# Performance work log

Hardware: AMD Instinct MI355X
Metric: run time of the kernel (lower is better)

The kernel has to match this reference:

```python
import jax, jax.numpy as jnp
import numpy as np

# module config (matches init_kwargs)
NUM_COL_HEADS = 4
NUM_ROW_HEADS = 4
EMBED_COL_DIM = 64
EMBED_ROW_DIM = 64
HEAD_COL = EMBED_COL_DIM // NUM_COL_HEADS  # 16
HEAD_ROW = EMBED_ROW_DIM // NUM_ROW_HEADS  # 16
SCALE = (HEAD_COL * HEAD_ROW) ** (-0.5)


def matrix_mul(x, u, v):
    # 'nm,blnd,dk->blmk'
    return jnp.einsum('nm,blnd,dk->blmk', u, x, v)


def setup_inputs() -> dict:
    key = jax.random.key(0)
    k1, k2, k3, k4, k5 = jax.random.split(key, 5)
    B, L, C, R = 2, 2048, 64, 64
    x = jax.random.normal(k1, (B, L, C, R), dtype=jnp.float32)
    qkv_u = jax.random.uniform(k2, (C, EMBED_COL_DIM), dtype=jnp.float32)
    qkv_v = jax.random.uniform(k3, (R, EMBED_ROW_DIM * 3), dtype=jnp.float32)
    proj_u = jax.random.uniform(k4, (EMBED_COL_DIM, C), dtype=jnp.float32)
    proj_v = jax.random.uniform(k5, (EMBED_ROW_DIM, R), dtype=jnp.float32)
    return {"x": x, "qkv_u": qkv_u, "qkv_v": qkv_v, "proj_u": proj_u, "proj_v": proj_v}


def reference(x, qkv_u, qkv_v, proj_u, proj_v):
    B, L, C, R = x.shape
    # bilinear QKV projection: [B,L,embed_col,3*embed_row]
    qkv = matrix_mul(x, qkv_u, qkv_v)
    qkv = qkv.reshape(B, L, 3, NUM_COL_HEADS, HEAD_COL, NUM_ROW_HEADS, HEAD_ROW)
    qkv = qkv.transpose(2, 0, 3, 5, 1, 4, 6)  # [3,B,Mc,Mr,L,Hc,Hw]
    q, k, v = qkv[0], qkv[1], qkv[2]
    # attention over combined (head_col, head_row) feature axes
    attn = jnp.einsum('bmnihw,bmnjhw->bmnij', q, k)
    attn = jax.nn.softmax(attn / SCALE, axis=-1)  # note: divides by scale, as in source
    out = jnp.einsum('bmnij,bmnjhw->bmnihw', attn, v)
    out = out.transpose(0, 3, 1, 4, 2, 5).reshape(B, L, EMBED_COL_DIM, EMBED_ROW_DIM)
    out = matrix_mul(out, proj_u, proj_v)
    return out
```

## Files before the change

kernel.cpp:

```cpp
#include <hip/hip_runtime.h>
#include <hip/hip_fp16.h>

typedef _Float16 f16x8 __attribute__((ext_vector_type(8)));
typedef _Float16 f16x4 __attribute__((ext_vector_type(4)));
typedef float f32x4 __attribute__((ext_vector_type(4)));


__device__ __forceinline__ void stage16(const _Float16* g, _Float16* l) {
  __builtin_amdgcn_global_load_lds(
      (const __attribute__((address_space(1))) void*)g,
      (__attribute__((address_space(3))) void*)l, 16, 0, 0);
}

__device__ __forceinline__ unsigned int pk2(float a, float b) {
  union { _Float16 h[2]; unsigned int u; } x;
  x.h[0] = (_Float16)a; x.h[1] = (_Float16)b;
  return x.u;
}

struct hl16 { _Float16 h, l; };
__device__ __forceinline__ hl16 split_f16(float v) {
  hl16 r;
  r.h = (_Float16)v;
  r.l = (_Float16)(v - (float)r.h);
  return r;
}

__global__ __launch_bounds__(256) void qkv_kernel(
    const float* __restrict__ x, const float* __restrict__ u,
    const float* __restrict__ v, _Float16* __restrict__ Q,
    _Float16* __restrict__ K, _Float16* __restrict__ V) {
  __shared__ _Float16 sm[24576];
  _Float16* xs_hi = sm;
  _Float16* xs_lo = sm + 4096;
  _Float16* us_hi = sm + 8192;
  _Float16* us_lo = sm + 12288;
  _Float16* Ts_hi = sm + 16384;
  _Float16* Ts_lo = sm + 20480;
  _Float16* vc_hi = sm;
  _Float16* vc_lo = sm + 7680;
  _Float16* qk16 = sm;
  const int bl = blockIdx.x;
  const int b = bl >> 11, l = bl & 2047;
  const int t = threadIdx.x;
  const int w = t >> 6, lane = t & 63;
  const int l15 = lane & 15, quad = lane >> 4;

  {
    const int d = t & 63, wq = t >> 6;
#pragma unroll
    for (int rr = 0; rr < 2; ++rr) {
      const int n0 = wq * 8 + rr * 32;
      f16x8 xh, xl, uh, ul;
#pragma unroll
      for (int j = 0; j < 8; ++j) {
        hl16 sx = split_f16(x[((size_t)bl << 12) + (n0 + j) * 64 + d]);
        hl16 su = split_f16(u[(n0 + j) * 64 + d]);
        xh[j] = sx.h; xl[j] = sx.l;
        uh[j] = su.h; ul[j] = su.l;
      }
      const int un = ((n0 >> 3) ^ (d & 7)) << 3;
      *(f16x8*)(xs_hi + (d << 6) + un) = xh;
      *(f16x8*)(xs_lo + (d << 6) + un) = xl;
      *(f16x8*)(us_hi + (d << 6) + un) = uh;
      *(f16x8*)(us_lo + (d << 6) + un) = ul;
    }
  }
  __syncthreads();

  {
    f32x4 dacc[4];
#pragma unroll
    for (int mt = 0; mt < 4; ++mt) dacc[mt] = (f32x4){0.f, 0.f, 0.f, 0.f};
    const int d = (w << 4) | l15;
#pragma unroll
    for (int ks = 0; ks < 2; ++ks) {
      const int ug = (((ks * 4 + quad) ^ (d & 7)) << 3);
      f16x8 bh = *(const f16x8*)(xs_hi + (d << 6) + ug);
      f16x8 blo = *(const f16x8*)(xs_lo + (d << 6) + ug);
#pragma unroll
      for (int mt = 0; mt < 4; ++mt) {
        const int m = (mt << 4) | l15;
        const int um = (((ks * 4 + quad) ^ (m & 7)) << 3);
        f16x8 ah = *(const f16x8*)(us_hi + (m << 6) + um);
        f16x8 al = *(const f16x8*)(us_lo + (m << 6) + um);
        dacc[mt] = __builtin_amdgcn_mfma_f32_16x16x32_f16(ah, bh, dacc[mt], 0, 0, 0);
        dacc[mt] = __builtin_amdgcn_mfma_f32_16x16x32_f16(ah, blo, dacc[mt], 0, 0, 0);
        dacc[mt] = __builtin_amdgcn_mfma_f32_16x16x32_f16(al, bh, dacc[mt], 0, 0, 0);
      }
    }
#pragma unroll
    for (int mt = 0; mt < 4; ++mt) {
#pragma unroll
      for (int r = 0; r < 4; ++r) {
        const int m = (mt << 4) | (quad << 2) | r;
        const int dd = (w << 4) | l15;
        const int off = (m << 6) + ((((dd >> 3) ^ (m & 7)) << 3) | (dd & 7));
        hl16 st = split_f16(dacc[mt][r]);
        Ts_hi[off] = st.h;
        Ts_lo[off] = st.l;
      }
    }
  }
  __syncthreads();

  f32x4 cacc[4][3];
#pragma unroll
  for (int mt = 0; mt < 4; ++mt)
#pragma unroll
    for (int kt = 0; kt < 3; ++kt) cacc[mt][kt] = (f32x4){0.f, 0.f, 0.f, 0.f};

  for (int chk = 0; chk < 2; ++chk) {
#pragma unroll
    for (int rr = 0; rr < 3; ++rr) {
      const int c768 = t + 256 * rr;
      const int k = c768 >> 2, sg = c768 & 3;
      f16x8 vh, vl;
#pragma unroll
      for (int j = 0; j < 8; ++j) {
        hl16 sv = split_f16(v[(chk * 32 + sg * 8 + j) * 192 + k]);
        vh[j] = sv.h; vl[j] = sv.l;
      }
      *(f16x8*)(vc_hi + k * 40 + sg * 8) = vh;
      *(f16x8*)(vc_lo + k * 40 + sg * 8) = vl;
    }
    __syncthreads();
    f16x8 ah[4], al[4];
#pragma unroll
    for (int mt = 0; mt < 4; ++mt) {
      const int m = (mt << 4) | l15;
      const int off = (m << 6) + (((chk * 4 + quad) ^ (m & 7)) << 3);
      ah[mt] = *(const f16x8*)(Ts_hi + off);
      al[mt] = *(const f16x8*)(Ts_lo + off);
    }
#pragma unroll
    for (int kt = 0; kt < 3; ++kt) {
      const int k = w * 48 + kt * 16 + l15;
      f16x8 bh = *(const f16x8*)(vc_hi + k * 40 + quad * 8);
      f16x8 blo = *(const f16x8*)(vc_lo + k * 40 + quad * 8);
#pragma unroll
      for (int mt = 0; mt < 4; ++mt) {
        cacc[mt][kt] = __builtin_amdgcn_mfma_f32_16x16x32_f16(ah[mt], bh, cacc[mt][kt], 0, 0, 0);
        cacc[mt][kt] = __builtin_amdgcn_mfma_f32_16x16x32_f16(ah[mt], blo, cacc[mt][kt], 0, 0, 0);
        cacc[mt][kt] = __builtin_amdgcn_mfma_f32_16x16x32_f16(al[mt], bh, cacc[mt][kt], 0, 0, 0);
      }
    }
    __syncthreads();
  }

#pragma unroll
  for (int mt = 0; mt < 4; ++mt)
#pragma unroll
    for (int kt = 0; kt < 3; ++kt) {
      const int k = w * 48 + kt * 16 + l15;
#pragma unroll
      for (int r = 0; r < 4; ++r) {
        const int m = (mt << 4) | (quad << 2) | r;
        qk16[m * 192 + k] = (_Float16)cacc[mt][kt][r];
      }
    }
  __syncthreads();

#pragma unroll
  for (int s = 0; s < 3; ++s) {
    const int rho = t + 256 * s;
    const int m = rho / 12, rem = rho - m * 12;
    const int k64 = rem >> 2, mr = rem & 3;
    const int chf = 3 * m + k64;
    const int t3 = chf >> 6, ch = chf & 63;
    const int f0 = (ch & 15) << 4;
    const int h = (b << 4) | ((ch >> 4) << 2) | mr;
    const _Float16* src = qk16 + m * 192 + k64 * 64 + mr * 16;
    f16x8 a0 = *(const f16x8*)src;
    f16x8 a1 = *(const f16x8*)(src + 8);
    _Float16* base = (t3 == 0) ? Q : (t3 == 1) ? K : V;
    _Float16* dst = base + (((size_t)h * 2048 + l) << 8) + f0;
    *(f16x8*)dst = a0;
    *(f16x8*)(dst + 8) = a1;
  }
}

__global__ __launch_bounds__(256) void vtrans_kernel(
    const _Float16* __restrict__ V, _Float16* __restrict__ Vt) {
  __shared__ _Float16 tb[64 * 72];
  const int bid = blockIdx.x;
  const int h = bid >> 7;
  const int lt = (bid >> 2) & 31;
  const int ft = bid & 3;
  const int l0 = lt << 6, f0 = ft << 6;
  const int t = threadIdx.x;
  const int r = t >> 2, s = (t & 3) << 4;
  const _Float16* src = V + (((size_t)h * 2048 + l0 + r) << 8) + f0 + s;
  *(f16x8*)(tb + r * 72 + s) = *(const f16x8*)src;
  *(f16x8*)(tb + r * 72 + s + 8) = *(const f16x8*)(src + 8);
  __syncthreads();
  _Float16 buf[16];
#pragma unroll
  for (int j = 0; j < 16; ++j) buf[j] = tb[(s + j) * 72 + r];
  _Float16* dst = Vt + (((size_t)(h << 8) + f0 + r) << 11) + l0 + s;
  *(f16x8*)dst = *(f16x8*)buf;
  *(f16x8*)(dst + 8) = *(f16x8*)(buf + 8);
}

__global__ __launch_bounds__(256, 2) void attn_kernel(
    const _Float16* __restrict__ Q, const _Float16* __restrict__ K,
    const _Float16* __restrict__ Vt, _Float16* __restrict__ O) {
  __shared__ _Float16 Ks[2][32 * 256];
  __shared__ _Float16 Vs[2][256 * 32];
  __shared__ unsigned int Ps[4 * 32 * 18];
  const int i = blockIdx.x;
  const int h = (i & 7) * 4 + (i >> 7);
  const int qt = (i >> 3) & 15;
  const int tid = threadIdx.x;
  const int w = tid >> 6, lane = tid & 63;
  const int l15 = lane & 15, quad = lane >> 4;
  const int q0 = qt * 128 + w * 32;

  const _Float16* Kt = K + (((size_t)h * 2048) << 8);
  const _Float16* Vtb = Vt + (((size_t)h << 8) << 11);

  f16x8 qf[2][8];
#pragma unroll
  for (int qh = 0; qh < 2; ++qh) {
    const _Float16* qb = Q + (((size_t)h * 2048 + q0 + qh * 16 + l15) << 8) + quad * 8;
#pragma unroll
    for (int kc = 0; kc < 8; ++kc) qf[qh][kc] = *(const f16x8*)(qb + kc * 32);
  }

  f32x4 oacc[2][16];
#pragma unroll
  for (int qh = 0; qh < 2; ++qh)
#pragma unroll
    for (int fb = 0; fb < 16; ++fb) oacc[qh][fb] = (f32x4){0.f, 0.f, 0.f, 0.f};
  float m2[2] = {-1e30f, -1e30f};
  float ell[2] = {0.f, 0.f};
  const float SC = 23.083120654223414f;

  auto stage_tile = [&](int kt, int bb) {
    const int k0 = kt * 32;
#pragma unroll
    for (int o = 0; o < 4; ++o) {
      const int c = tid + o * 256;
      const int row = c >> 5, unit = c & 31;
      stage16(Kt + (((size_t)(k0 + row)) << 8) + ((unit ^ (row & 7)) << 3),
              &Ks[bb][c * 8]);
      const int g = c >> 3, ip = c & 7;
      const int sl = (g << 3) | (ip ^ (g & 7));
      const int f = sl >> 2, ku = sl & 3;
      stage16(Vtb + (((size_t)f) << 11) + k0 + ku * 8, &Vs[bb][c * 8]);
    }
  };

  unsigned int* pw = Ps + w * 32 * 18;
  stage_tile(0, 0);
  for (int kt = 0; kt < 64; ++kt) {
    const int cb = kt & 1;
    if (kt < 63) {
      stage_tile(kt + 1, cb ^ 1);
      asm volatile("s_waitcnt vmcnt(8)" ::: "memory");
    } else {
      asm volatile("s_waitcnt vmcnt(0)" ::: "memory");
    }
    __builtin_amdgcn_s_barrier();
    asm volatile("" ::: "memory");

    f32x4 c00 = {0.f, 0.f, 0.f, 0.f}, c01 = c00, c10 = c00, c11 = c00;
#pragma unroll
    for (int kc = 0; kc < 8; ++kc) {
      const int u0 = ((kc * 4 + quad) ^ (l15 & 7)) << 3;
      f16x8 kf0 = *(const f16x8*)(&Ks[cb][l15 * 256 + u0]);
      f16x8 kf1 = *(const f16x8*)(&Ks[cb][(16 + l15) * 256 + u0]);
      c00 = __builtin_amdgcn_mfma_f32_16x16x32_f16(kf0, qf[0][kc], c00, 0, 0, 0);
      c01 = __builtin_amdgcn_mfma_f32_16x16x32_f16(kf0, qf[1][kc], c01, 0, 0, 0);
      c10 = __builtin_amdgcn_mfma_f32_16x16x32_f16(kf1, qf[0][kc], c10, 0, 0, 0);
      c11 = __builtin_amdgcn_mfma_f32_16x16x32_f16(kf1, qf[1][kc], c11, 0, 0, 0);
    }

    float alpha[2];
    bool upd = false;
#pragma unroll
    for (int qh = 0; qh < 2; ++qh) {
      const f32x4 ck0 = qh ? c01 : c00;
      const f32x4 ck1 = qh ? c11 : c10;
      float s0[4], s1[4];
#pragma unroll
      for (int r = 0; r < 4; ++r) { s0[r] = ck0[r] * SC; s1[r] = ck1[r] * SC; }
      float mx = fmaxf(fmaxf(fmaxf(s0[0], s0[1]), fmaxf(s0[2], s0[3])),
                       fmaxf(fmaxf(s1[0], s1[1]), fmaxf(s1[2], s1[3])));
      mx = fmaxf(mx, __shfl_xor(mx, 16));
      mx = fmaxf(mx, __shfl_xor(mx, 32));
      const float mo = m2[qh];
      const bool u8 = (mx > mo + 8.f);
      const float mn = u8 ? mx : mo;
      m2[qh] = mn;
      upd |= u8;
      const float a = exp2f(mo - mn);
      alpha[qh] = a;
      float p0[4], p1[4];
#pragma unroll
      for (int r = 0; r < 4; ++r) { p0[r] = exp2f(s0[r] - mn); p1[r] = exp2f(s1[r] - mn); }
      ell[qh] = ell[qh] * a + ((p0[0] + p0[1]) + (p0[2] + p0[3])) +
                ((p1[0] + p1[1]) + (p1[2] + p1[3]));
      unsigned int* row = pw + (qh * 16 + l15) * 18;
      row[quad * 2 + 0] = pk2(p0[0], p0[1]);
      row[quad * 2 + 1] = pk2(p0[2], p0[3]);
      row[8 + quad * 2 + 0] = pk2(p1[0], p1[1]);
      row[8 + quad * 2 + 1] = pk2(p1[2], p1[3]);
    }
    if (__any(upd)) {
#pragma unroll
      for (int qh = 0; qh < 2; ++qh)
#pragma unroll
        for (int fb = 0; fb < 16; ++fb) oacc[qh][fb] *= alpha[qh];
    }
    f16x8 pf[2];
#pragma unroll
    for (int qh = 0; qh < 2; ++qh) {
      const _Float16* pr = (const _Float16*)(pw + (qh * 16 + l15) * 18);
      union { f16x8 v; f16x4 h[2]; } tmp;
      tmp.h[0] = *(const f16x4*)(pr + quad * 8);
      tmp.h[1] = *(const f16x4*)(pr + quad * 8 + 4);
      pf[qh] = tmp.v;
    }
#pragma unroll
    for (int fb = 0; fb < 16; ++fb) {
      const int f = fb * 16 + l15;
      const int g = f >> 1;
      const int ip = (((f & 1) << 2) | quad) ^ (g & 7);
      f16x8 vf = *(const f16x8*)(&Vs[cb][(((g << 3) | ip)) * 8]);
      oacc[0][fb] = __builtin_amdgcn_mfma_f32_16x16x32_f16(vf, pf[0], oacc[0][fb], 0, 0, 0);
      oacc[1][fb] = __builtin_amdgcn_mfma_f32_16x16x32_f16(vf, pf[1], oacc[1][fb], 0, 0, 0);
    }
    asm volatile("" ::: "memory");
    __builtin_amdgcn_s_barrier();
  }

#pragma unroll
  for (int qh = 0; qh < 2; ++qh) {
    float e = ell[qh];
    e += __shfl_xor(e, 16);
    e += __shfl_xor(e, 32);
    const float inv = 1.f / e;
    _Float16* ob = O + (((size_t)h * 2048 + q0 + qh * 16 + l15) << 8) + quad * 4;
#pragma unroll
    for (int fb = 0; fb < 16; ++fb) {
      f16x4 ov;
#pragma unroll
      for (int r = 0; r < 4; ++r) ov[r] = (_Float16)(oacc[qh][fb][r] * inv);
      *(f16x4*)(ob + fb * 16) = ov;
    }
  }
}

__global__ __launch_bounds__(256) void proj_kernel(
    const _Float16* __restrict__ O, const float* __restrict__ pu,
    const float* __restrict__ pv, float* __restrict__ out) {
  __shared__ _Float16 sm[20480];
  _Float16* os = sm;
  _Float16* put_hi = sm + 4096;
  _Float16* put_lo = sm + 8192;
  _Float16* pvt_hi = sm + 12288;
  _Float16* pvt_lo = sm + 16384;
  _Float16* gt_hi = sm;
  _Float16* gt_lo = sm + 12288;
  const int bl = blockIdx.x;
  const int b = bl >> 11, l = bl & 2047;
  const int t = threadIdx.x;
  const int w = t >> 6, lane = t & 63;
  const int l15 = lane & 15, quad = lane >> 4;

  {
    const int hh = t >> 4, hc = t & 15;
    const int mc = hh >> 2, mr = hh & 3;
    const int hg = (b << 4) | hh;
    const _Float16* src = O + (((size_t)hg * 2048 + l) << 8) + hc * 16;
    const int n = mc * 16 + hc, d0 = mr * 16;
    f16x8 v0 = *(const f16x8*)(src);
    f16x8 v1 = *(const f16x8*)(src + 8);
    *(f16x8*)(os + (n << 6) + ((((d0 >> 3) + 0) ^ (n & 7)) << 3)) = v0;
    *(f16x8*)(os + (n << 6) + ((((d0 >> 3) + 1) ^ (n & 7)) << 3)) = v1;
  }
  {
    const int c = t & 63, wq = t >> 6;
#pragma unroll
    for (int rr = 0; rr < 2; ++rr) {
      const int r0 = wq * 8 + rr * 32;
      f16x8 uh, ul, vh, vl;
#pragma unroll
      for (int j = 0; j < 8; ++j) {
        hl16 su = split_f16(pu[(r0 + j) * 64 + c]);
        hl16 sv = split_f16(pv[(r0 + j) * 64 + c]);
        uh[j] = su.h; ul[j] = su.l;
        vh[j] = sv.h; vl[j] = sv.l;
      }
      const int un = ((r0 >> 3) ^ (c & 7)) << 3;
      *(f16x8*)(put_hi + (c << 6) + un) = uh;
      *(f16x8*)(put_lo + (c << 6) + un) = ul;
      *(f16x8*)(pvt_hi + (c << 6) + un) = vh;
      *(f16x8*)(pvt_lo + (c << 6) + un) = vl;
    }
  }
  __syncthreads();

  f32x4 gacc[4];
#pragma unroll
  for (int nt = 0; nt < 4; ++nt) gacc[nt] = (f32x4){0.f, 0.f, 0.f, 0.f};
  {
    const int k = (w << 4) | l15;
#pragma unroll
    for (int ks = 0; ks < 2; ++ks) {
      const int uk = (((ks * 4 + quad) ^ (k & 7)) << 3);
      f16x8 bh = *(const f16x8*)(pvt_hi + (k << 6) + uk);
      f16x8 blo = *(const f16x8*)(pvt_lo + (k << 6) + uk);
#pragma unroll
      for (int nt = 0; nt < 4; ++nt) {
        const int n = (nt << 4) | l15;
        const int un = (((ks * 4 + quad) ^ (n & 7)) << 3);
        f16x8 a = *(const f16x8*)(os + (n << 6) + un);
        gacc[nt] = __builtin_amdgcn_mfma_f32_16x16x32_f16(a, bh, gacc[nt], 0, 0, 0);
        gacc[nt] = __builtin_amdgcn_mfma_f32_16x16x32_f16(a, blo, gacc[nt], 0, 0, 0);
      }
    }
  }
  __syncthreads();
  {
    const int k = (w << 4) | l15;
#pragma unroll
    for (int nt = 0; nt < 4; ++nt) {
#pragma unroll
      for (int r = 0; r < 4; ++r) {
        const int n = (nt << 4) | (quad << 2) | r;
        const int off = (k << 6) + ((((n >> 3) ^ (k & 7)) << 3) | (n & 7));
        hl16 sg = split_f16(gacc[nt][r]);
        gt_hi[off] = sg.h;
        gt_lo[off] = sg.l;
      }
    }
  }
  __syncthreads();

  {
    f32x4 cacc[4];
#pragma unroll
    for (int mt = 0; mt < 4; ++mt) cacc[mt] = (f32x4){0.f, 0.f, 0.f, 0.f};
    const int k = (w << 4) | l15;
#pragma unroll
    for (int ks = 0; ks < 2; ++ks) {
      const int uk = (((ks * 4 + quad) ^ (k & 7)) << 3);
      f16x8 bh = *(const f16x8*)(gt_hi + (k << 6) + uk);
      f16x8 blo = *(const f16x8*)(gt_lo + (k << 6) + uk);
#pragma unroll
      for (int mt = 0; mt < 4; ++mt) {
        const int m = (mt << 4) | l15;
        const int um = (((ks * 4 + quad) ^ (m & 7)) << 3);
        f16x8 ah = *(const f16x8*)(put_hi + (m << 6) + um);
        f16x8 al = *(const f16x8*)(put_lo + (m << 6) + um);
        cacc[mt] = __builtin_amdgcn_mfma_f32_16x16x32_f16(ah, bh, cacc[mt], 0, 0, 0);
        cacc[mt] = __builtin_amdgcn_mfma_f32_16x16x32_f16(ah, blo, cacc[mt], 0, 0, 0);
        cacc[mt] = __builtin_amdgcn_mfma_f32_16x16x32_f16(al, bh, cacc[mt], 0, 0, 0);
      }
    }
    float* og = out + ((size_t)bl << 12);
#pragma unroll
    for (int mt = 0; mt < 4; ++mt) {
#pragma unroll
      for (int r = 0; r < 4; ++r) {
        const int m = (mt << 4) | (quad << 2) | r;
        og[m * 64 + k] = cacc[mt][r];
      }
    }
  }
}

extern "C" void kernel_launch(void* const* d_in, const int* in_sizes, int n_in,
                              void* d_out, int out_size, void* d_ws, size_t ws_size,
                              hipStream_t stream) {
  (void)in_sizes; (void)n_in; (void)out_size; (void)ws_size;
  const float* x = (const float*)d_in[0];
  const float* u = (const float*)d_in[1];
  const float* v = (const float*)d_in[2];
  const float* pu = (const float*)d_in[3];
  const float* pv = (const float*)d_in[4];
  const size_t SEG = (size_t)32 * 2048 * 256;
  _Float16* Q = (_Float16*)d_ws;
  _Float16* K = Q + SEG;
  _Float16* Vt = K + SEG;
  _Float16* O = Vt + SEG;
  _Float16* V = O;
  qkv_kernel<<<4096, 256, 0, stream>>>(x, u, v, Q, K, V);
  vtrans_kernel<<<4096, 256, 0, stream>>>(V, Vt);
  attn_kernel<<<512, 256, 0, stream>>>(Q, K, Vt, O);
  proj_kernel<<<4096, 256, 0, stream>>>(O, pu, pv, (float*)d_out);
}
```

Measured before the change: 420.1 us.

## Single-buffer V tile, shuffle P in registers, raise occupancy to three blocks

The V shared-memory tile goes from double to single buffering. V for the next tile is now staged after the end-of-iteration barrier, so it overlaps the next QK^T phase instead of a whole iteration. The P matrix is transposed across lanes with __shfl rather than written to and read back from an LDS scratch buffer. The LDS savings allow launch bounds to request three blocks per SIMD group instead of two, for more latency hiding. The cost is less prefetch slack for V, extra shuffle instructions, and tighter register limits that may cause spills given the large accumulator array.

New measurement: 922.6 us. 2.2x slower.

```diff
diff --git a/kernel.cpp b/kernel.cpp
--- a/kernel.cpp
+++ b/kernel.cpp
@@ -202,12 +202,11 @@
   *(f16x8*)(dst + 8) = *(f16x8*)(buf + 8);
 }
 
-__global__ __launch_bounds__(256, 2) void attn_kernel(
+__global__ __launch_bounds__(256, 3) void attn_kernel(
     const _Float16* __restrict__ Q, const _Float16* __restrict__ K,
     const _Float16* __restrict__ Vt, _Float16* __restrict__ O) {
   __shared__ _Float16 Ks[2][32 * 256];
-  __shared__ _Float16 Vs[2][256 * 32];
-  __shared__ unsigned int Ps[4 * 32 * 18];
+  __shared__ _Float16 Vs[256 * 32];
   const int i = blockIdx.x;
   const int h = (i & 7) * 4 + (i >> 7);
   const int qt = (i >> 3) & 15;
@@ -236,7 +235,7 @@
   float ell[2] = {0.f, 0.f};
   const float SC = 23.083120654223414f;
 
-  auto stage_tile = [&](int kt, int bb) {
+  auto stage_K = [&](int kt, int bb) {
     const int k0 = kt * 32;
 #pragma unroll
     for (int o = 0; o < 4; ++o) {
@@ -244,20 +243,27 @@
       const int row = c >> 5, unit = c & 31;
       stage16(Kt + (((size_t)(k0 + row)) << 8) + ((unit ^ (row & 7)) << 3),
               &Ks[bb][c * 8]);
+    }
+  };
+  auto stage_V = [&](int kt) {
+    const int k0 = kt * 32;
+#pragma unroll
+    for (int o = 0; o < 4; ++o) {
+      const int c = tid + o * 256;
       const int g = c >> 3, ip = c & 7;
       const int sl = (g << 3) | (ip ^ (g & 7));
       const int f = sl >> 2, ku = sl & 3;
-      stage16(Vtb + (((size_t)f) << 11) + k0 + ku * 8, &Vs[bb][c * 8]);
+      stage16(Vtb + (((size_t)f) << 11) + k0 + ku * 8, &Vs[c * 8]);
     }
   };
 
-  unsigned int* pw = Ps + w * 32 * 18;
-  stage_tile(0, 0);
+  stage_K(0, 0);
+  stage_V(0);
   for (int kt = 0; kt < 64; ++kt) {
     const int cb = kt & 1;
     if (kt < 63) {
-      stage_tile(kt + 1, cb ^ 1);
-      asm volatile("s_waitcnt vmcnt(8)" ::: "memory");
+      stage_K(kt + 1, cb ^ 1);
+      asm volatile("s_waitcnt vmcnt(4)" ::: "memory");
     } else {
       asm volatile("s_waitcnt vmcnt(0)" ::: "memory");
     }
@@ -277,6 +283,7 @@
     }
 
     float alpha[2];
+    unsigned int pA0[2], pA1[2], pB0[2], pB1[2];
     bool upd = false;
 #pragma unroll
     for (int qh = 0; qh < 2; ++qh) {
@@ -301,11 +308,10 @@
       for (int r = 0; r < 4; ++r) { p0[r] = exp2f(s0[r] - mn); p1[r] = exp2f(s1[r] - mn); }
       ell[qh] = ell[qh] * a + ((p0[0] + p0[1]) + (p0[2] + p0[3])) +
                 ((p1[0] + p1[1]) + (p1[2] + p1[3]));
-      unsigned int* row = pw + (qh * 16 + l15) * 18;
-      row[quad * 2 + 0] = pk2(p0[0], p0[1]);
-      row[quad * 2 + 1] = pk2(p0[2], p0[3]);
-      row[8 + quad * 2 + 0] = pk2(p1[0], p1[1]);
-      row[8 + quad * 2 + 1] = pk2(p1[2], p1[3]);
+      pA0[qh] = pk2(p0[0], p0[1]);
+      pA1[qh] = pk2(p0[2], p0[3]);
+      pB0[qh] = pk2(p1[0], p1[1]);
+      pB1[qh] = pk2(p1[2], p1[3]);
     }
     if (__any(upd)) {
 #pragma unroll
@@ -314,25 +320,37 @@
         for (int fb = 0; fb < 16; ++fb) oacc[qh][fb] *= alpha[qh];
     }
     f16x8 pf[2];
-#pragma unroll
-    for (int qh = 0; qh < 2; ++qh) {
-      const _Float16* pr = (const _Float16*)(pw + (qh * 16 + l15) * 18);
-      union { f16x8 v; f16x4 h[2]; } tmp;
-      tmp.h[0] = *(const f16x4*)(pr + quad * 8);
-      tmp.h[1] = *(const f16x4*)(pr + quad * 8 + 4);
-      pf[qh] = tmp.v;
+    {
+      const int srcLo = ((quad & 1) << 5) | l15;
+      const int srcHi = srcLo + 16;
+      const bool hi = (quad >> 1) != 0;
+#pragma unroll
+      for (int qh = 0; qh < 2; ++qh) {
+        unsigned int a0 = __shfl(pA0[qh], srcLo), b0 = __shfl(pB0[qh], srcLo);
+        unsigned int a1 = __shfl(pA1[qh], srcLo), b1 = __shfl(pB1[qh], srcLo);
+        unsigned int a2 = __shfl(pA0[qh], srcHi), b2 = __shfl(pB0[qh], srcHi);
+        unsigned int a3 = __shfl(pA1[qh], srcHi), b3 = __shfl(pB1[qh], srcHi);
+        union { f16x8 v; unsigned int d[4]; } tp;
+        tp.d[0] = hi ? b0 : a0;
+        tp.d[1] = hi ? b1 : a1;
+        tp.d[2] = hi ? b2 : a2;
+        tp.d[3] = hi ? b3 : a3;
+        pf[qh] = tp.v;
+      }
     }
 #pragma unroll
     for (int fb = 0; fb < 16; ++fb) {
       const int f = fb * 16 + l15;
       const int g = f >> 1;
       const int ip = (((f & 1) << 2) | quad) ^ (g & 7);
-      f16x8 vf = *(const f16x8*)(&Vs[cb][(((g << 3) | ip)) * 8]);
+      f16x8 vf = *(const f16x8*)(&Vs[(((g << 3) | ip)) * 8]);
       oacc[0][fb] = __builtin_amdgcn_mfma_f32_16x16x32_f16(vf, pf[0], oacc[0][fb], 0, 0, 0);
       oacc[1][fb] = __builtin_amdgcn_mfma_f32_16x16x32_f16(vf, pf[1], oacc[1][fb], 0, 0, 0);
     }
     asm volatile("" ::: "memory");
     __builtin_amdgcn_s_barrier();
+    asm volatile("" ::: "memory");
+    if (kt < 63) stage_V(kt + 1);
   }
 
 #pragma unroll
```
